# Kernel tuning notes

Measured on AMD Instinct MI355X. Metric: run time of the kernel, lower is better.

## Reference

```python
import jax, jax.numpy as jnp
import numpy as np

N_P, N_S, N_D = 100000, 2000, 3
C_P, C_S, C_D = 128, 64, 16
HID, HEADS, NCLS = 128, 4, 3
E_HAS, E_BEL, E_SIM = 300000, 100000, 400000
BN_EPS = 1e-5

def _segment_softmax(alpha, seg, num_segments):
    # PyG-style softmax over destination segments: exp(a - max) / (sum + 1e-16)
    amax = jax.ops.segment_max(alpha, seg, num_segments=num_segments)
    amax = jnp.where(jnp.isfinite(amax), amax, 0.0)
    e = jnp.exp(alpha - amax[seg])
    denom = jax.ops.segment_sum(e, seg, num_segments=num_segments)
    return e / (denom[seg] + 1e-16)

def _han_edge(x_src, x_dst, ei, a_src, a_dst, num_dst):
    # x_*: [N, H, D]; a_*: [H, D]; ei: [2, E]. GAT-style per-edge-type attention.
    s, d = ei[0], ei[1]
    al_s = jnp.einsum('nhd,hd->nh', x_src, a_src)
    al_d = jnp.einsum('nhd,hd->nh', x_dst, a_dst)
    alpha = jax.nn.leaky_relu(al_s[s] + al_d[d], 0.2)      # [E, H]
    w = _segment_softmax(alpha, d, num_dst)
    msg = x_src[s] * w[:, :, None]                          # [E, H, D]
    out = jax.ops.segment_sum(msg, d, num_segments=num_dst)
    H, D = a_src.shape
    return jax.nn.relu(out.reshape(num_dst, H * D))

def _han_layer(x_p, x_s, x_d, ei_has, ei_bel, ei_sim,
               wp, bp, ws, bs, wd, bd,
               a_sh, a_dh, a_sb, a_db, a_ss, a_ds, heads, out_ch):
    D = out_ch // heads
    hp = (x_p @ wp.T + bp).reshape(-1, heads, D)
    hs = (x_s @ ws.T + bs).reshape(-1, heads, D)
    hd = (x_d @ wd.T + bd).reshape(-1, heads, D)
    out_s = _han_edge(hp, hs, ei_has, a_sh, a_dh, hs.shape[0])
    out_d = _han_edge(hp, hd, ei_bel, a_sb, a_db, hd.shape[0])
    out_p = _han_edge(hp, hp, ei_sim, a_ss, a_ds, hp.shape[0])
    # Semantic attention (group): each dst type receives exactly one metapath
    # here, so softmax over a single score is identically 1 and fusion is the
    # identity -- the semantic q/k_lin params have no numerical effect.
    return out_p, out_s, out_d

def reference(x_patient, x_symptom, x_dosha, ei_has, ei_bel, ei_sim,
              w1_patient, b1_patient, w1_symptom, b1_symptom, w1_dosha, b1_dosha,
              a1_src_has, a1_dst_has, a1_src_bel, a1_dst_bel, a1_src_sim, a1_dst_sim,
              bn_w, bn_b, bn_mean, bn_var,
              w2_patient, b2_patient, w2_symptom, b2_symptom, w2_dosha, b2_dosha,
              a2_src_has, a2_dst_has, a2_src_bel, a2_dst_bel, a2_src_sim, a2_dst_sim):
    op, os_, od = _han_layer(x_patient, x_symptom, x_dosha, ei_has, ei_bel, ei_sim,
                             w1_patient, b1_patient, w1_symptom, b1_symptom, w1_dosha, b1_dosha,
                             a1_src_has, a1_dst_has, a1_src_bel, a1_dst_bel,
                             a1_src_sim, a1_dst_sim, HEADS, HID)
    # eval-mode BatchNorm1d shared across node types, then ELU (dropout = id in eval)
    inv = bn_w / jnp.sqrt(bn_var + BN_EPS)
    bn_elu = lambda v: jax.nn.elu((v - bn_mean) * inv + bn_b)
    op, os_, od = bn_elu(op), bn_elu(os_), bn_elu(od)
    op2, _, _ = _han_layer(op, os_, od, ei_has, ei_bel, ei_sim,
                           w2_patient, b2_patient, w2_symptom, b2_symptom, w2_dosha, b2_dosha,
                           a2_src_has, a2_dst_has, a2_src_bel, a2_dst_bel,
                           a2_src_sim, a2_dst_sim, 1, NCLS)
    return jax.nn.log_softmax(op2, axis=1)

def setup_inputs():
    key = jax.random.key(0)
    ks = list(jax.random.split(key, 32))
    nrm = lambda k, shp, s: jax.random.normal(k, shp, jnp.float32) * s
    ri = lambda k, n, hi: jax.random.randint(k, (n,), 0, hi, dtype=jnp.int32)
    D1 = HID // HEADS
    inp = {}
    inp['x_patient'] = nrm(ks[0], (N_P, C_P), 1.0)
    inp['x_symptom'] = nrm(ks[1], (N_S, C_S), 1.0)
    inp['x_dosha'] = nrm(ks[2], (N_D, C_D), 1.0)
    inp['ei_has'] = jnp.stack([ri(ks[3], E_HAS, N_P), ri(ks[4], E_HAS, N_S)])
    inp['ei_bel'] = jnp.stack([ri(ks[5], E_BEL, N_P), ri(ks[6], E_BEL, N_D)])
    inp['ei_sim'] = jnp.stack([ri(ks[7], E_SIM, N_P), ri(ks[8], E_SIM, N_P)])
    inp['w1_patient'] = nrm(ks[9], (HID, C_P), 0.05); inp['b1_patient'] = jnp.zeros(HID)
    inp['w1_symptom'] = nrm(ks[10], (HID, C_S), 0.05); inp['b1_symptom'] = jnp.zeros(HID)
    inp['w1_dosha'] = nrm(ks[11], (HID, C_D), 0.05); inp['b1_dosha'] = jnp.zeros(HID)
    inp['a1_src_has'] = nrm(ks[12], (HEADS, D1), 0.1); inp['a1_dst_has'] = nrm(ks[13], (HEADS, D1), 0.1)
    inp['a1_src_bel'] = nrm(ks[14], (HEADS, D1), 0.1); inp['a1_dst_bel'] = nrm(ks[15], (HEADS, D1), 0.1)
    inp['a1_src_sim'] = nrm(ks[16], (HEADS, D1), 0.1); inp['a1_dst_sim'] = nrm(ks[17], (HEADS, D1), 0.1)
    inp['bn_w'] = jnp.ones(HID); inp['bn_b'] = jnp.zeros(HID)
    inp['bn_mean'] = jnp.zeros(HID); inp['bn_var'] = jnp.ones(HID)
    inp['w2_patient'] = nrm(ks[18], (NCLS, HID), 0.05); inp['b2_patient'] = jnp.zeros(NCLS)
    inp['w2_symptom'] = nrm(ks[19], (NCLS, HID), 0.05); inp['b2_symptom'] = jnp.zeros(NCLS)
    inp['w2_dosha'] = nrm(ks[20], (NCLS, HID), 0.05); inp['b2_dosha'] = jnp.zeros(NCLS)
    inp['a2_src_has'] = nrm(ks[21], (1, NCLS), 0.1); inp['a2_dst_has'] = nrm(ks[22], (1, NCLS), 0.1)
    inp['a2_src_bel'] = nrm(ks[23], (1, NCLS), 0.1); inp['a2_dst_bel'] = nrm(ks[24], (1, NCLS), 0.1)
    inp['a2_src_sim'] = nrm(ks[25], (1, NCLS), 0.1); inp['a2_dst_sim'] = nrm(ks[26], (1, NCLS), 0.1)
    return inp
```

## Files before the change

### kernel.cpp

```cpp
#include <hip/hip_runtime.h>
#include <hip/hip_bf16.h>

typedef float f32x4 __attribute__((ext_vector_type(4)));
typedef float f32x2 __attribute__((ext_vector_type(2)));
typedef unsigned short u16x4 __attribute__((ext_vector_type(4)));
typedef unsigned short u16x8 __attribute__((ext_vector_type(8)));
typedef short bf16x8 __attribute__((ext_vector_type(8)));

#define HID 128
#define RT  4
#define ELLW 32

__device__ __forceinline__ float b2f(unsigned short u) {
    return __uint_as_float(((unsigned int)u) << 16);
}
__device__ __forceinline__ unsigned short f2b(float f) {
    unsigned int u = __float_as_uint(f);
    unsigned int r = (u + 0x7FFFu + ((u >> 16) & 1u)) >> 16;
    return (unsigned short)r;
}

__device__ __forceinline__ bool detect_f32(const unsigned short* xp) {
    int sane = 0;
#pragma unroll
    for (int i = 0; i < 16; ++i) {
        int ex = (xp[2 * i] >> 7) & 0xFF;
        sane += (ex >= 120 && ex <= 130);
    }
    return sane < 8;
}
__device__ __forceinline__ bool detect_i64(const int* ei) {
    return (ei[1] | ei[3] | ei[5] | ei[7]) == 0;
}
__device__ __forceinline__ float ldf(const unsigned short* p, long i, bool f32) {
    return f32 ? ((const float*)p)[i] : b2f(p[i]);
}
__device__ __forceinline__ f32x4 ld4(const unsigned short* p, int c0, bool f32) {
    if (f32) return *(const f32x4*)((const float*)p + c0);
    u16x4 q = *(const u16x4*)(p + c0);
    return (f32x4){b2f(q[0]), b2f(q[1]), b2f(q[2]), b2f(q[3])};
}
__device__ __forceinline__ int ei_at(const int* ei, long idx, bool i64) {
    return i64 ? ei[2 * idx] : ei[idx];
}
__device__ __forceinline__ float lrelu(float a) {
    return a > 0.f ? a : 0.2f * a;
}

__global__ __launch_bounds__(256) void gemm1_scat_k(
    const unsigned short* __restrict__ x,
    const unsigned short* __restrict__ w,
    const unsigned short* __restrict__ bias,
    const unsigned short* __restrict__ a1s,
    const unsigned short* __restrict__ a1d,
    unsigned short* __restrict__ hp,
    float* __restrict__ al_s, float* __restrict__ al_d, int n_rows,
    const int* __restrict__ ei, int E,
    int* __restrict__ cursor, int* __restrict__ csrc, int gb, int sb)
{
    const int bid = (int)blockIdx.x;
    const int sb3 = 3 * sb;
    if (bid < sb3 && (bid % 3) == 2) {
        const bool i64 = detect_i64(ei);
        const int nth = sb * 256;
        const int idx = (bid / 3) * 256 + (int)threadIdx.x;
        int s[4], d[4], pos[4]; bool v[4];
#pragma unroll
        for (int k = 0; k < 4; ++k) {
            int e = idx + k * nth;
            v[k] = e < E;
            if (v[k]) {
                s[k] = ei_at(ei, e, i64);
                d[k] = ei_at(ei, (long)E + e, i64);
            }
        }
#pragma unroll
        for (int k = 0; k < 4; ++k)
            if (v[k]) pos[k] = atomicAdd(&cursor[d[k]], 1);
#pragma unroll
        for (int k = 0; k < 4; ++k)
            if (v[k]) csrc[(d[k] << 5) + pos[k]] = s[k];
        return;
    }
    const int gidx = (bid < sb3) ? (bid - (bid + 1) / 3) : (bid - sb);
    if (gidx >= gb) return;

    const bool f32m = detect_f32(x);
    const int wave  = threadIdx.x >> 6;
    const int lane  = threadIdx.x & 63;
    const int nhalf = wave & 1;
    const int rtile = wave >> 1;
    const int m     = lane & 15;
    const int quad  = lane >> 4;

    bf16x8 wfrag[4][4];
#pragma unroll
    for (int ks = 0; ks < 4; ++ks)
#pragma unroll
        for (int nt = 0; nt < 4; ++nt) {
            int col = nhalf * 64 + nt * 16 + m;
            if (!f32m) {
                wfrag[ks][nt] = *(const bf16x8*)(w + (long)col * HID + ks * 32 + quad * 8);
            } else {
                const float* wf = (const float*)w;
#pragma unroll
                for (int j = 0; j < 8; ++j)
                    wfrag[ks][nt][j] = (short)f2b(wf[(long)col * HID + ks * 32 + quad * 8 + j]);
            }
        }

    f32x4 bb[4], as4[4], ad4[4];
#pragma unroll
    for (int nt = 0; nt < 4; ++nt) {
        const int c0 = nhalf * 64 + nt * 16 + quad * 4;
        bb[nt]  = ld4(bias, c0, f32m);
        as4[nt] = ld4(a1s,  c0, f32m);
        ad4[nt] = ld4(a1d,  c0, f32m);
    }

    const long base = (long)gidx * (32 * RT);

#pragma unroll
    for (int tt = 0; tt < RT; ++tt) {
        const long row0 = base + tt * 32 + rtile * 16;
        if (row0 >= n_rows) break;
        const long row = row0 + m;

        bf16x8 afrag[4];
        {
            long arow = row < n_rows ? row : n_rows - 1;
            if (!f32m) {
#pragma unroll
                for (int ks = 0; ks < 4; ++ks)
                    afrag[ks] = *(const bf16x8*)(x + arow * HID + ks * 32 + quad * 8);
            } else {
                const float* xf = (const float*)x;
#pragma unroll
                for (int ks = 0; ks < 4; ++ks)
#pragma unroll
                    for (int j = 0; j < 8; ++j)
                        afrag[ks][j] = (short)f2b(xf[arow * HID + ks * 32 + quad * 8 + j]);
            }
        }

        f32x4 acc[4];
#pragma unroll
        for (int nt = 0; nt < 4; ++nt) acc[nt] = (f32x4){0.f, 0.f, 0.f, 0.f};
#pragma unroll
        for (int nt = 0; nt < 4; ++nt)
#pragma unroll
            for (int ks = 0; ks < 4; ++ks)
                acc[nt] = __builtin_amdgcn_mfma_f32_16x16x32_bf16(
                    wfrag[ks][nt], afrag[ks], acc[nt], 0, 0, 0);

        float als_p[2] = {0.f, 0.f}, ald_p[2] = {0.f, 0.f};
#pragma unroll
        for (int nt = 0; nt < 4; ++nt) {
            const int c0 = nhalf * 64 + nt * 16 + quad * 4;
            float v0 = acc[nt][0] + bb[nt][0];
            float v1 = acc[nt][1] + bb[nt][1];
            float v2 = acc[nt][2] + bb[nt][2];
            float v3 = acc[nt][3] + bb[nt][3];
            if (row < n_rows) {
                u16x4 st = {f2b(v0), f2b(v1), f2b(v2), f2b(v3)};
                *(u16x4*)(hp + row * HID + c0) = st;
            }
            const int hl = nt >> 1;
            als_p[hl] += v0 * as4[nt][0] + v1 * as4[nt][1] + v2 * as4[nt][2] + v3 * as4[nt][3];
            ald_p[hl] += v0 * ad4[nt][0] + v1 * ad4[nt][1] + v2 * ad4[nt][2] + v3 * ad4[nt][3];
        }
#pragma unroll
        for (int off = 16; off < 64; off <<= 1) {
            als_p[0] += __shfl_xor(als_p[0], off);
            als_p[1] += __shfl_xor(als_p[1], off);
            ald_p[0] += __shfl_xor(ald_p[0], off);
            ald_p[1] += __shfl_xor(ald_p[1], off);
        }
        if (quad == 0 && row < n_rows) {
            const int hb = nhalf * 2;
            *(f32x2*)(al_s + row * 4 + hb) = (f32x2){als_p[0], als_p[1]};
            *(f32x2*)(al_d + row * 4 + hb) = (f32x2){ald_p[0], ald_p[1]};
        }
    }
}

__global__ __launch_bounds__(256) void msg1_fused_k(
    const int* __restrict__ degc,
    const int* __restrict__ csrc,
    const unsigned short* __restrict__ hp,
    const float* __restrict__ al_s, const float* __restrict__ al_d,
    const unsigned short* __restrict__ bn_w, const unsigned short* __restrict__ bn_b,
    const unsigned short* __restrict__ bn_m, const unsigned short* __restrict__ bn_v,
    const unsigned short* __restrict__ w2,   const unsigned short* __restrict__ b2,
    const unsigned short* __restrict__ a2s,  const unsigned short* __restrict__ a2d,
    const unsigned short* __restrict__ xp,
    float* __restrict__ hp2, float* __restrict__ al2d,
    int n_p)
{
    const bool f32m = detect_f32(xp);
    __shared__ float s_inv[128], s_mu[128], s_beta[128];
    __shared__ float s_w2[3][128];
    __shared__ float s_scal[9];
    {
        int t = threadIdx.x;
        if (t < 128) {
            float bw = ldf(bn_w, t, f32m), bv = ldf(bn_v, t, f32m);
            s_inv[t]  = bw / sqrtf(bv + 1e-5f);
            s_mu[t]   = ldf(bn_m, t, f32m);
            s_beta[t] = ldf(bn_b, t, f32m);
            s_w2[0][t] = ldf(w2, 0 * HID + t, f32m);
            s_w2[1][t] = ldf(w2, 1 * HID + t, f32m);
            s_w2[2][t] = ldf(w2, 2 * HID + t, f32m);
        } else if (t < 131) {
            int k = t - 128;
            s_scal[k]     = ldf(b2, k, f32m);
            s_scal[3 + k] = ldf(a2s, k, f32m);
            s_scal[6 + k] = ldf(a2d, k, f32m);
        }
    }
    __syncthreads();

    const int lt = threadIdx.x & 15;
    const int d  = blockIdx.x * 16 + (threadIdx.x >> 4);
    if (d >= n_p) return;
    const int h = lt >> 2;
    const float ald = al_d[(long)d * 4 + h];
    const int deg = degc[d];
    const int beg = d << 5, end = beg + deg;
    const int niter = (deg + 3) >> 2;

    float dsum = 0.f;
    float acc[8] = {0.f,0.f,0.f,0.f,0.f,0.f,0.f,0.f};
    int p = beg;
    for (int it = 0; it < niter; ++it, p += 4) {
        int s0 = csrc[p + 0], s1 = csrc[p + 1], s2 = csrc[p + 2], s3 = csrc[p + 3];
        unsigned u0 = (unsigned)s0 < (unsigned)n_p ? (unsigned)s0 : 0u;
        unsigned u1 = (unsigned)s1 < (unsigned)n_p ? (unsigned)s1 : 0u;
        unsigned u2 = (unsigned)s2 < (unsigned)n_p ? (unsigned)s2 : 0u;
        unsigned u3 = (unsigned)s3 < (unsigned)n_p ? (unsigned)s3 : 0u;
        float a0 = al_s[(long)u0 * 4 + h];
        float a1 = al_s[(long)u1 * 4 + h];
        float a2 = al_s[(long)u2 * 4 + h];
        float a3 = al_s[(long)u3 * 4 + h];
        u16x8 v0 = *(const u16x8*)(hp + (long)u0 * HID + lt * 8);
        u16x8 v1 = *(const u16x8*)(hp + (long)u1 * HID + lt * 8);
        u16x8 v2 = *(const u16x8*)(hp + (long)u2 * HID + lt * 8);
        u16x8 v3 = *(const u16x8*)(hp + (long)u3 * HID + lt * 8);
        float w0 = (p + 0 < end) ? __expf(lrelu(a0 + ald)) : 0.f;
        float w1 = (p + 1 < end) ? __expf(lrelu(a1 + ald)) : 0.f;
        float w2_ = (p + 2 < end) ? __expf(lrelu(a2 + ald)) : 0.f;
        float w3 = (p + 3 < end) ? __expf(lrelu(a3 + ald)) : 0.f;
        dsum += (w0 + w1) + (w2_ + w3);
#pragma unroll
        for (int k = 0; k < 8; ++k)
            acc[k] += b2f(v0[k]) * w0 + b2f(v1[k]) * w1
                    + b2f(v2[k]) * w2_ + b2f(v3[k]) * w3;
    }

    const float r = 1.f / (dsum + 1e-16f);
    float p0 = 0.f, p1 = 0.f, p2 = 0.f;
#pragma unroll
    for (int k = 0; k < 8; ++k) {
        int j = lt * 8 + k;
        float v = acc[k] * r;
        v = v > 0.f ? v : 0.f;
        v = (v - s_mu[j]) * s_inv[j] + s_beta[j];
        v = v > 0.f ? v : (__expf(v) - 1.f);
        p0 += v * s_w2[0][j];
        p1 += v * s_w2[1][j];
        p2 += v * s_w2[2][j];
    }
#pragma unroll
    for (int msk = 8; msk; msk >>= 1) {
        p0 += __shfl_xor(p0, msk);
        p1 += __shfl_xor(p1, msk);
        p2 += __shfl_xor(p2, msk);
    }
    if (lt == 0) {
        p0 += s_scal[0]; p1 += s_scal[1]; p2 += s_scal[2];
        float a2sv = p0 * s_scal[3] + p1 * s_scal[4] + p2 * s_scal[5];
        *(f32x4*)(hp2 + (long)d * 4) = (f32x4){p0, p1, p2, a2sv};
        al2d[d] = p0 * s_scal[6] + p1 * s_scal[7] + p2 * s_scal[8];
    }
}

__global__ __launch_bounds__(256) void l2final_k(
    const int* __restrict__ degc,
    const int* __restrict__ csrc,
    const float* __restrict__ hp2,
    const float* __restrict__ al2d,
    const unsigned short* __restrict__ xp,
    void* __restrict__ out, int n_p)
{
    const bool f32m = detect_f32(xp);
    const int t  = blockIdx.x * 256 + threadIdx.x;
    const int d  = t >> 2;
    const int sl = t & 3;
    if (d >= n_p) return;
    const int beg = d << 5, end = beg + degc[d];
    const float ald = al2d[d];

    float a0s = 0.f, a1s = 0.f, a2s_ = 0.f, ds = 0.f;
    for (int p = beg + sl; p < end; p += 4) {
        int s = csrc[p];
        f32x4 hv = *(const f32x4*)(hp2 + (long)s * 4);
        float w = __expf(lrelu(hv[3] + ald));
        ds += w;
        a0s += hv[0] * w; a1s += hv[1] * w; a2s_ += hv[2] * w;
    }
#pragma unroll
    for (int off = 1; off < 4; off <<= 1) {
        ds  += __shfl_xor(ds, off);
        a0s += __shfl_xor(a0s, off);
        a1s += __shfl_xor(a1s, off);
        a2s_ += __shfl_xor(a2s_, off);
    }
    if (sl != 0) return;

    const float r = 1.f / (ds + 1e-16f);
    float v0 = fmaxf(a0s * r, 0.f);
    float v1 = fmaxf(a1s * r, 0.f);
    float v2 = fmaxf(a2s_ * r, 0.f);
    float m = fmaxf(v0, fmaxf(v1, v2));
    float lse = m + __logf(__expf(v0 - m) + __expf(v1 - m) + __expf(v2 - m));
    if (f32m) {
        float* o = (float*)out;
        o[(long)d * 3 + 0] = v0 - lse;
        o[(long)d * 3 + 1] = v1 - lse;
        o[(long)d * 3 + 2] = v2 - lse;
    } else {
        __hip_bfloat16* o = (__hip_bfloat16*)out;
        o[(long)d * 3 + 0] = __float2bfloat16(v0 - lse);
        o[(long)d * 3 + 1] = __float2bfloat16(v1 - lse);
        o[(long)d * 3 + 2] = __float2bfloat16(v2 - lse);
    }
}

extern "C" void kernel_launch(void* const* d_in, const int* in_sizes, int n_in,
                              void* d_out, int out_size, void* d_ws, size_t ws_size,
                              hipStream_t stream)
{
    const unsigned short* x_p = (const unsigned short*)d_in[0];
    const int*            ei  = (const int*)d_in[5];
    const unsigned short* w1p = (const unsigned short*)d_in[6];
    const unsigned short* b1p = (const unsigned short*)d_in[7];
    const unsigned short* a1s = (const unsigned short*)d_in[16];
    const unsigned short* a1d = (const unsigned short*)d_in[17];
    const unsigned short* bnw = (const unsigned short*)d_in[18];
    const unsigned short* bnb = (const unsigned short*)d_in[19];
    const unsigned short* bnm = (const unsigned short*)d_in[20];
    const unsigned short* bnv = (const unsigned short*)d_in[21];
    const unsigned short* w2p = (const unsigned short*)d_in[22];
    const unsigned short* b2p = (const unsigned short*)d_in[23];
    const unsigned short* a2s = (const unsigned short*)d_in[32];
    const unsigned short* a2d = (const unsigned short*)d_in[33];

    const int n_p   = in_sizes[0] / HID;
    const int e_sim = in_sizes[5] / 2;

    float* ws = (float*)d_ws;
    size_t o = 0;
    int* cursor = (int*)(ws + o);                     o += (size_t)n_p;
    size_t zlen = o;
    int* csrc   = (int*)(ws + o);                     o += (size_t)n_p * ELLW;
    unsigned short* hp = (unsigned short*)(ws + o);   o += (size_t)n_p * HID / 2;
    float* al_s = ws + o;                             o += (size_t)n_p * 4;
    float* al_d = ws + o;                             o += (size_t)n_p * 4;
    float* hp2  = ws + o;                             o += (size_t)n_p * 4;
    float* al2d = ws + o;                             o += (size_t)n_p;

    hipMemsetAsync((void*)ws, 0, zlen * sizeof(float), stream);

    const int gb = (n_p + 32 * RT - 1) / (32 * RT);
    const int sb = (e_sim + 4 * 256 - 1) / (4 * 256);
    gemm1_scat_k<<<gb + sb, 256, 0, stream>>>(
        x_p, w1p, b1p, a1s, a1d, hp, al_s, al_d, n_p, ei, e_sim, cursor, csrc, gb, sb);

    msg1_fused_k<<<(n_p + 15) / 16, 256, 0, stream>>>(cursor, csrc, hp, al_s, al_d,
                                                      bnw, bnb, bnm, bnv, w2p, b2p,
                                                      a2s, a2d, x_p,
                                                      hp2, al2d, n_p);

    l2final_k<<<((long)n_p * 4 + 255) / 256, 256, 0, stream>>>(
        cursor, csrc, hp2, al2d, x_p, d_out, n_p);
}
```

Baseline: 234.0 us.

## Fuse all stages into one persistent cooperative kernel with grid syncs

Replaces the memset plus three separate launches with one cooperative persistent kernel. It zeroes the cursor array, runs the GEMM/edge-scatter phase, the first-layer message aggregation and the final layer in sequence, separated by grid.sync. The aim is to remove launch gaps and the memset. In exchange the grid is capped at around 1024 blocks, grid barriers add cost, and per-block smem setup is repeated. The old multi-kernel path remains as a fallback if the cooperative launch fails.

Measured after the change: 671.2 us. 187% more time.

```diff
diff --git a/kernel.cpp b/kernel.cpp
--- a/kernel.cpp
+++ b/kernel.cpp
@@ -1,5 +1,8 @@
 #include <hip/hip_runtime.h>
 #include <hip/hip_bf16.h>
+#include <hip/hip_cooperative_groups.h>
+
+namespace cg = cooperative_groups;
 
 typedef float f32x4 __attribute__((ext_vector_type(4)));
 typedef float f32x2 __attribute__((ext_vector_type(2)));
@@ -45,6 +48,297 @@
 }
 __device__ __forceinline__ float lrelu(float a) {
     return a > 0.f ? a : 0.2f * a;
+}
+
+__global__ __launch_bounds__(256, 4) void all_k(
+    const unsigned short* __restrict__ x,
+    const unsigned short* __restrict__ w,
+    const unsigned short* __restrict__ bias,
+    const unsigned short* __restrict__ a1s,
+    const unsigned short* __restrict__ a1d,
+    unsigned short* __restrict__ hp,
+    float* __restrict__ al_s, float* __restrict__ al_d, int n_p,
+    const int* __restrict__ ei, int E,
+    int* __restrict__ cursor, int* __restrict__ csrc, int gb, int sb,
+    const unsigned short* __restrict__ bn_w, const unsigned short* __restrict__ bn_b,
+    const unsigned short* __restrict__ bn_m, const unsigned short* __restrict__ bn_v,
+    const unsigned short* __restrict__ w2,   const unsigned short* __restrict__ b2,
+    const unsigned short* __restrict__ pa2s, const unsigned short* __restrict__ pa2d,
+    float* __restrict__ hp2, float* __restrict__ al2d,
+    void* __restrict__ out)
+{
+    cg::grid_group grid = cg::this_grid();
+    const int NB  = (int)gridDim.x;
+    const int tid = (int)threadIdx.x;
+    const bool f32m = detect_f32(x);
+
+    __shared__ float s_inv[128], s_mu[128], s_beta[128];
+    __shared__ float s_w2[3][128];
+    __shared__ float s_scal[9];
+    if (tid < 128) {
+        float bw = ldf(bn_w, tid, f32m), bv = ldf(bn_v, tid, f32m);
+        s_inv[tid]  = bw / sqrtf(bv + 1e-5f);
+        s_mu[tid]   = ldf(bn_m, tid, f32m);
+        s_beta[tid] = ldf(bn_b, tid, f32m);
+        s_w2[0][tid] = ldf(w2, 0 * HID + tid, f32m);
+        s_w2[1][tid] = ldf(w2, 1 * HID + tid, f32m);
+        s_w2[2][tid] = ldf(w2, 2 * HID + tid, f32m);
+    } else if (tid < 131) {
+        int k = tid - 128;
+        s_scal[k]     = ldf(b2, k, f32m);
+        s_scal[3 + k] = ldf(pa2s, k, f32m);
+        s_scal[6 + k] = ldf(pa2d, k, f32m);
+    }
+    __syncthreads();
+
+    for (int i = (int)blockIdx.x * 256 + tid; i < n_p; i += NB * 256)
+        cursor[i] = 0;
+    __threadfence();
+    grid.sync();
+
+    const int sb3 = 3 * sb;
+    for (int bid = (int)blockIdx.x; bid < gb + sb; bid += NB) {
+        if (bid < sb3 && (bid % 3) == 2) {
+            const bool i64 = detect_i64(ei);
+            const int nth = sb * 256;
+            const int idx = (bid / 3) * 256 + tid;
+            int s[4], d[4], pos[4]; bool v[4];
+#pragma unroll
+            for (int k = 0; k < 4; ++k) {
+                int e = idx + k * nth;
+                v[k] = e < E;
+                if (v[k]) {
+                    s[k] = ei_at(ei, e, i64);
+                    d[k] = ei_at(ei, (long)E + e, i64);
+                }
+            }
+#pragma unroll
+            for (int k = 0; k < 4; ++k)
+                if (v[k]) pos[k] = atomicAdd(&cursor[d[k]], 1);
+#pragma unroll
+            for (int k = 0; k < 4; ++k)
+                if (v[k]) csrc[(d[k] << 5) + pos[k]] = s[k];
+            continue;
+        }
+        const int gidx = (bid < sb3) ? (bid - (bid + 1) / 3) : (bid - sb);
+        if (gidx >= gb) continue;
+
+        const int wave  = tid >> 6;
+        const int lane  = tid & 63;
+        const int nhalf = wave & 1;
+        const int rtile = wave >> 1;
+        const int m     = lane & 15;
+        const int quad  = lane >> 4;
+
+        bf16x8 wfrag[4][4];
+#pragma unroll
+        for (int ks = 0; ks < 4; ++ks)
+#pragma unroll
+            for (int nt = 0; nt < 4; ++nt) {
+                int col = nhalf * 64 + nt * 16 + m;
+                if (!f32m) {
+                    wfrag[ks][nt] = *(const bf16x8*)(w + (long)col * HID + ks * 32 + quad * 8);
+                } else {
+                    const float* wf = (const float*)w;
+#pragma unroll
+                    for (int j = 0; j < 8; ++j)
+                        wfrag[ks][nt][j] = (short)f2b(wf[(long)col * HID + ks * 32 + quad * 8 + j]);
+                }
+            }
+
+        f32x4 bb[4], as4[4], ad4[4];
+#pragma unroll
+        for (int nt = 0; nt < 4; ++nt) {
+            const int c0 = nhalf * 64 + nt * 16 + quad * 4;
+            bb[nt]  = ld4(bias, c0, f32m);
+            as4[nt] = ld4(a1s,  c0, f32m);
+            ad4[nt] = ld4(a1d,  c0, f32m);
+        }
+
+        const long base = (long)gidx * (32 * RT);
+
+#pragma unroll
+        for (int tt = 0; tt < RT; ++tt) {
+            const long row0 = base + tt * 32 + rtile * 16;
+            if (row0 >= n_p) break;
+            const long row = row0 + m;
+
+            bf16x8 afrag[4];
+            {
+                long arow = row < n_p ? row : n_p - 1;
+                if (!f32m) {
+#pragma unroll
+                    for (int ks = 0; ks < 4; ++ks)
+                        afrag[ks] = *(const bf16x8*)(x + arow * HID + ks * 32 + quad * 8);
+                } else {
+                    const float* xf = (const float*)x;
+#pragma unroll
+                    for (int ks = 0; ks < 4; ++ks)
+#pragma unroll
+                        for (int j = 0; j < 8; ++j)
+                            afrag[ks][j] = (short)f2b(xf[arow * HID + ks * 32 + quad * 8 + j]);
+                }
+            }
+
+            f32x4 acc[4];
+#pragma unroll
+            for (int nt = 0; nt < 4; ++nt) acc[nt] = (f32x4){0.f, 0.f, 0.f, 0.f};
+#pragma unroll
+            for (int nt = 0; nt < 4; ++nt)
+#pragma unroll
+                for (int ks = 0; ks < 4; ++ks)
+                    acc[nt] = __builtin_amdgcn_mfma_f32_16x16x32_bf16(
+                        wfrag[ks][nt], afrag[ks], acc[nt], 0, 0, 0);
+
+            float als_p[2] = {0.f, 0.f}, ald_p[2] = {0.f, 0.f};
+#pragma unroll
+            for (int nt = 0; nt < 4; ++nt) {
+                const int c0 = nhalf * 64 + nt * 16 + quad * 4;
+                float v0 = acc[nt][0] + bb[nt][0];
+                float v1 = acc[nt][1] + bb[nt][1];
+                float v2 = acc[nt][2] + bb[nt][2];
+                float v3 = acc[nt][3] + bb[nt][3];
+                if (row < n_p) {
+                    u16x4 st = {f2b(v0), f2b(v1), f2b(v2), f2b(v3)};
+                    *(u16x4*)(hp + row * HID + c0) = st;
+                }
+                const int hl = nt >> 1;
+                als_p[hl] += v0 * as4[nt][0] + v1 * as4[nt][1] + v2 * as4[nt][2] + v3 * as4[nt][3];
+                ald_p[hl] += v0 * ad4[nt][0] + v1 * ad4[nt][1] + v2 * ad4[nt][2] + v3 * ad4[nt][3];
+            }
+#pragma unroll
+            for (int off = 16; off < 64; off <<= 1) {
+                als_p[0] += __shfl_xor(als_p[0], off);
+                als_p[1] += __shfl_xor(als_p[1], off);
+                ald_p[0] += __shfl_xor(ald_p[0], off);
+                ald_p[1] += __shfl_xor(ald_p[1], off);
+            }
+            if (quad == 0 && row < n_p) {
+                const int hb = nhalf * 2;
+                *(f32x2*)(al_s + row * 4 + hb) = (f32x2){als_p[0], als_p[1]};
+                *(f32x2*)(al_d + row * 4 + hb) = (f32x2){ald_p[0], ald_p[1]};
+            }
+        }
+    }
+    __threadfence();
+    grid.sync();
+
+    {
+        const int lt = tid & 15;
+        const int h  = lt >> 2;
+        const int nvb = (n_p + 15) / 16;
+        for (int vb = (int)blockIdx.x; vb < nvb; vb += NB) {
+            const int d = vb * 16 + (tid >> 4);
+            if (d >= n_p) continue;
+            const float ald = al_d[(long)d * 4 + h];
+            const int deg = cursor[d];
+            const int beg = d << 5, end = beg + deg;
+            const int niter = (deg + 3) >> 2;
+
+            float dsum = 0.f;
+            float acc[8] = {0.f,0.f,0.f,0.f,0.f,0.f,0.f,0.f};
+            int p = beg;
+            for (int it = 0; it < niter; ++it, p += 4) {
+                int s0 = csrc[p + 0], s1 = csrc[p + 1], s2 = csrc[p + 2], s3 = csrc[p + 3];
+                unsigned u0 = (unsigned)s0 < (unsigned)n_p ? (unsigned)s0 : 0u;
+                unsigned u1 = (unsigned)s1 < (unsigned)n_p ? (unsigned)s1 : 0u;
+                unsigned u2 = (unsigned)s2 < (unsigned)n_p ? (unsigned)s2 : 0u;
+                unsigned u3 = (unsigned)s3 < (unsigned)n_p ? (unsigned)s3 : 0u;
+                float a0 = al_s[(long)u0 * 4 + h];
+                float a1 = al_s[(long)u1 * 4 + h];
+                float a2 = al_s[(long)u2 * 4 + h];
+                float a3 = al_s[(long)u3 * 4 + h];
+                u16x8 v0 = *(const u16x8*)(hp + (long)u0 * HID + lt * 8);
+                u16x8 v1 = *(const u16x8*)(hp + (long)u1 * HID + lt * 8);
+                u16x8 v2 = *(const u16x8*)(hp + (long)u2 * HID + lt * 8);
+                u16x8 v3 = *(const u16x8*)(hp + (long)u3 * HID + lt * 8);
+                float w0 = (p + 0 < end) ? __expf(lrelu(a0 + ald)) : 0.f;
+                float w1 = (p + 1 < end) ? __expf(lrelu(a1 + ald)) : 0.f;
+                float w2_ = (p + 2 < end) ? __expf(lrelu(a2 + ald)) : 0.f;
+                float w3 = (p + 3 < end) ? __expf(lrelu(a3 + ald)) : 0.f;
+                dsum += (w0 + w1) + (w2_ + w3);
+#pragma unroll
+                for (int k = 0; k < 8; ++k)
+                    acc[k] += b2f(v0[k]) * w0 + b2f(v1[k]) * w1
+                            + b2f(v2[k]) * w2_ + b2f(v3[k]) * w3;
+            }
+
+            const float r = 1.f / (dsum + 1e-16f);
+            float p0 = 0.f, p1 = 0.f, p2 = 0.f;
+#pragma unroll
+            for (int k = 0; k < 8; ++k) {
+                int j = lt * 8 + k;
+                float v = acc[k] * r;
+                v = v > 0.f ? v : 0.f;
+                v = (v - s_mu[j]) * s_inv[j] + s_beta[j];
+                v = v > 0.f ? v : (__expf(v) - 1.f);
+                p0 += v * s_w2[0][j];
+                p1 += v * s_w2[1][j];
+                p2 += v * s_w2[2][j];
+            }
+#pragma unroll
+            for (int msk = 8; msk; msk >>= 1) {
+                p0 += __shfl_xor(p0, msk);
+                p1 += __shfl_xor(p1, msk);
+                p2 += __shfl_xor(p2, msk);
+            }
+            if (lt == 0) {
+                p0 += s_scal[0]; p1 += s_scal[1]; p2 += s_scal[2];
+                float a2v = p0 * s_scal[3] + p1 * s_scal[4] + p2 * s_scal[5];
+                *(f32x4*)(hp2 + (long)d * 4) = (f32x4){p0, p1, p2, a2v};
+                al2d[d] = p0 * s_scal[6] + p1 * s_scal[7] + p2 * s_scal[8];
+            }
+        }
+    }
+    __threadfence();
+    grid.sync();
+
+    {
+        const int nvb = (n_p * 4 + 255) / 256;
+        for (int vb = (int)blockIdx.x; vb < nvb; vb += NB) {
+            const int t  = vb * 256 + tid;
+            const int d  = t >> 2;
+            const int sl = t & 3;
+            if (d >= n_p) continue;
+            const int beg = d << 5, end = beg + cursor[d];
+            const float ald = al2d[d];
+
+            float a0s = 0.f, a1s_ = 0.f, a2s_ = 0.f, ds = 0.f;
+            for (int p = beg + sl; p < end; p += 4) {
+                int s = csrc[p];
+                f32x4 hv = *(const f32x4*)(hp2 + (long)s * 4);
+                float wv = __expf(lrelu(hv[3] + ald));
+                ds += wv;
+                a0s += hv[0] * wv; a1s_ += hv[1] * wv; a2s_ += hv[2] * wv;
+            }
+#pragma unroll
+            for (int off = 1; off < 4; off <<= 1) {
+                ds   += __shfl_xor(ds, off);
+                a0s  += __shfl_xor(a0s, off);
+                a1s_ += __shfl_xor(a1s_, off);
+                a2s_ += __shfl_xor(a2s_, off);
+            }
+            if (sl != 0) continue;
+
+            const float r = 1.f / (ds + 1e-16f);
+            float v0 = fmaxf(a0s * r, 0.f);
+            float v1 = fmaxf(a1s_ * r, 0.f);
+            float v2 = fmaxf(a2s_ * r, 0.f);
+            float mm = fmaxf(v0, fmaxf(v1, v2));
+            float lse = mm + __logf(__expf(v0 - mm) + __expf(v1 - mm) + __expf(v2 - mm));
+            if (f32m) {
+                float* o = (float*)out;
+                o[(long)d * 3 + 0] = v0 - lse;
+                o[(long)d * 3 + 1] = v1 - lse;
+                o[(long)d * 3 + 2] = v2 - lse;
+            } else {
+                __hip_bfloat16* o = (__hip_bfloat16*)out;
+                o[(long)d * 3 + 0] = __float2bfloat16(v0 - lse);
+                o[(long)d * 3 + 1] = __float2bfloat16(v1 - lse);
+                o[(long)d * 3 + 2] = __float2bfloat16(v2 - lse);
+            }
+        }
+    }
 }
 
 __global__ __launch_bounds__(256) void gemm1_scat_k(
@@ -344,19 +638,19 @@
     const int*            ei  = (const int*)d_in[5];
     const unsigned short* w1p = (const unsigned short*)d_in[6];
     const unsigned short* b1p = (const unsigned short*)d_in[7];
-    const unsigned short* a1s = (const unsigned short*)d_in[16];
-    const unsigned short* a1d = (const unsigned short*)d_in[17];
+    const unsigned short* a1sp = (const unsigned short*)d_in[16];
+    const unsigned short* a1dp = (const unsigned short*)d_in[17];
     const unsigned short* bnw = (const unsigned short*)d_in[18];
     const unsigned short* bnb = (const unsigned short*)d_in[19];
     const unsigned short* bnm = (const unsigned short*)d_in[20];
     const unsigned short* bnv = (const unsigned short*)d_in[21];
     const unsigned short* w2p = (const unsigned short*)d_in[22];
     const unsigned short* b2p = (const unsigned short*)d_in[23];
-    const unsigned short* a2s = (const unsigned short*)d_in[32];
-    const unsigned short* a2d = (const unsigned short*)d_in[33];
-
-    const int n_p   = in_sizes[0] / HID;
-    const int e_sim = in_sizes[5] / 2;
+    const unsigned short* a2sp = (const unsigned short*)d_in[32];
+    const unsigned short* a2dp = (const unsigned short*)d_in[33];
+
+    int n_p   = in_sizes[0] / HID;
+    int e_sim = in_sizes[5] / 2;
 
     float* ws = (float*)d_ws;
     size_t o = 0;
@@ -369,18 +663,35 @@
     float* hp2  = ws + o;                             o += (size_t)n_p * 4;
     float* al2d = ws + o;                             o += (size_t)n_p;
 
+    int gb = (n_p + 32 * RT - 1) / (32 * RT);
+    int sb = (e_sim + 4 * 256 - 1) / (4 * 256);
+
+    int bpc = 0;
+    hipError_t qerr = hipOccupancyMaxActiveBlocksPerMultiprocessor(&bpc, all_k, 256, 0);
+    int nb = (qerr == hipSuccess && bpc > 0) ? bpc * 256 : 512;
+    if (nb > 1024) nb = 1024;
+
+    void* args[] = {
+        (void*)&x_p, (void*)&w1p, (void*)&b1p, (void*)&a1sp, (void*)&a1dp,
+        (void*)&hp, (void*)&al_s, (void*)&al_d, (void*)&n_p,
+        (void*)&ei, (void*)&e_sim, (void*)&cursor, (void*)&csrc,
+        (void*)&gb, (void*)&sb,
+        (void*)&bnw, (void*)&bnb, (void*)&bnm, (void*)&bnv,
+        (void*)&w2p, (void*)&b2p, (void*)&a2sp, (void*)&a2dp,
+        (void*)&hp2, (void*)&al2d, (void*)&d_out
+    };
+    hipError_t lerr = hipLaunchCooperativeKernel((const void*)all_k,
+                                                 dim3(nb), dim3(256),
+                                                 args, 0, stream);
+    if (lerr == hipSuccess) return;
+
     hipMemsetAsync((void*)ws, 0, zlen * sizeof(float), stream);
-
-    const int gb = (n_p + 32 * RT - 1) / (32 * RT);
-    const int sb = (e_sim + 4 * 256 - 1) / (4 * 256);
     gemm1_scat_k<<<gb + sb, 256, 0, stream>>>(
-        x_p, w1p, b1p, a1s, a1d, hp, al_s, al_d, n_p, ei, e_sim, cursor, csrc, gb, sb);
-
+        x_p, w1p, b1p, a1sp, a1dp, hp, al_s, al_d, n_p, ei, e_sim, cursor, csrc, gb, sb);
     msg1_fused_k<<<(n_p + 15) / 16, 256, 0, stream>>>(cursor, csrc, hp, al_s, al_d,
                                                       bnw, bnb, bnm, bnv, w2p, b2p,
-                                                      a2s, a2d, x_p,
+                                                      a2sp, a2dp, x_p,
                                                       hp2, al2d, n_p);
-
     l2final_k<<<((long)n_p * 4 + 255) / 256, 256, 0, stream>>>(
         cursor, csrc, hp2, al2d, x_p, d_out, n_p);
 }
```
